# Kernel tuning notes

Hardware: AMD Instinct MI355X
Metric: run time of the kernel (lower is better)

The kernel has to match this reference:

```python
import jax, jax.numpy as jnp
import numpy as np
from jax.scipy.linalg import solve_triangular

# Production config from MFAWrapper.from_path: 28x28 images, 50 components, 6 factors
B, DFT, K, L = 2048, 784, 50, 6
LOG2PI = float(np.log(2.0 * np.pi))


def setup_inputs() -> dict:
    key = jax.random.key(0)
    k1, k2, k3, k4, k5, k6 = jax.random.split(key, 6)
    X = jax.random.normal(k1, (B, DFT), dtype=jnp.float32)
    J = jax.random.randint(k2, (B, DFT), 0, 2).astype(jnp.int32)  # binary observation mask
    MU = jax.random.normal(k3, (K, DFT), dtype=jnp.float32) * 0.5
    A_fac = jax.random.normal(k4, (K, DFT, L), dtype=jnp.float32) * 0.1  # factor loadings
    log_D = jax.random.normal(k5, (K, DFT), dtype=jnp.float32) * 0.1 - 1.0  # log noise variances
    PI_logits = jax.random.normal(k6, (K,), dtype=jnp.float32)
    return {"X": X, "J": J, "MU": MU, "A_fac": A_fac, "log_D": log_D, "PI_logits": PI_logits}


def _mfa_conditional(X, J, MU, A_fac, log_D, PI_logits):
    """Batched MFA conditional reconstruction given observed features (mask J==1).

    The per-sample torch.nonzero selection is replaced by mask-weighted linear
    algebra: restricting to observed rows of diag(1/D) is identical to zeroing
    the unobserved entries of the weight, so all B samples are conditioned in
    one batched pass instead of a Python loop.
    """
    dtype = X.dtype
    l = A_fac.shape[-1]
    Jf = (J == 1).astype(dtype)                 # [B, Dft]
    inv_D = jnp.exp(-log_D)                     # [K, Dft]
    # masked residual per (sample, component): [B, K, Dft]
    md = (X[:, None, :] - MU[None, :, :]) * Jf[:, None, :]
    # latent posterior precision P = I + A_o^T D_o^{-1} A_o  -> [B, K, L, L]
    P = jnp.einsum('bd,kd,kdi,kdj->bkij', Jf, inv_D, A_fac, A_fac) + jnp.eye(l, dtype=dtype)
    # q = A_o^T D_o^{-1} (x_o - mu_o)  -> [B, K, L]
    q = jnp.einsum('bkd,kd,kdi->bki', md, inv_D, A_fac)
    # per-component log-likelihood of observed features via Woodbury / matrix det lemma
    Lc = jnp.linalg.cholesky(P)                                         # [B, K, L, L]
    y = solve_triangular(Lc, q[..., None], lower=True)[..., 0]          # [B, K, L]
    quad = jnp.einsum('bkd,kd->bk', md * md, inv_D) - jnp.sum(y * y, axis=-1)
    logdet = (2.0 * jnp.sum(jnp.log(jnp.diagonal(Lc, axis1=-2, axis2=-1)), axis=-1)
              + jnp.einsum('bd,kd->bk', Jf, log_D))
    n_obs = jnp.sum(Jf, axis=-1, keepdims=True)                         # [B, 1]
    log_lik = -0.5 * (quad + logdet + n_obs * LOG2PI)                   # [B, K]
    log_resp = jax.nn.log_softmax(PI_logits)[None, :] + log_lik
    c = jnp.argmax(log_resp, axis=-1)                                   # most responsible component, [B]
    # gather per-sample selected component and form the conditional Gaussian in factor form
    P_sel = jnp.take_along_axis(P, c[:, None, None, None], axis=1)[:, 0]  # [B, L, L]
    q_sel = jnp.take_along_axis(q, c[:, None, None], axis=1)[:, 0]        # [B, L]
    A_sel = A_fac[c]                                                      # [B, Dft, L]
    m_z = jnp.linalg.solve(P_sel, q_sel[..., None])[..., 0]               # posterior latent mean [B, L]
    cov_z = jnp.linalg.inv(P_sel)                                         # posterior latent cov [B, L, L]
    Lz = jnp.linalg.cholesky(cov_z)
    M = MU[c] + jnp.einsum('bdi,bi->bd', A_sel, m_z)                      # conditional mean over all features
    A_out = jnp.einsum('bdi,bij->bdj', A_sel, Lz)                         # loadings: cond cov = A_out A_out^T + diag(D_out)
    D_out = jnp.exp(log_D)[c]                                             # [B, Dft]
    Pw = jnp.ones((X.shape[0], 1), dtype)
    return Pw, M, A_out, D_out


def reference(X, J, MU, A_fac, log_D, PI_logits):
    return _mfa_conditional(X, J, MU, A_fac, log_D, PI_logits)
```

## Files before the change

kernel.cpp:

```cpp
#include <hip/hip_runtime.h>
#include <math.h>

#define B_N 2048
#define D_FT 784
#define K_N 50
#define L_N 6
#define LOG2PI_F 1.8378770664093453f

#define OUT_PW 0
#define OUT_M  (B_N)
#define OUT_A  (OUT_M + B_N*D_FT)
#define OUT_D  (OUT_A + B_N*D_FT*6)

#define WS_SCORES 0
#define WS_PQ     (WS_SCORES + K_N*B_N)
#define WS_C      (WS_PQ + K_N*27*B_N)
#define WS_MZLZ   (WS_C + B_N)
#define WS_XT     (WS_MZLZ + B_N*28)
#define WS_JBT    (WS_XT + D_FT*B_N)

#define IDX(i,j) ((i)*((i)+1)/2 + (j))

typedef float v2f __attribute__((ext_vector_type(2)));

#define PK_FMA(acc, a, b) asm("v_pk_fma_f32 %0, %1, %2, %0" : "+v"(acc) : "v"(a), "v"(b))
#define PK_MUL(dst, a, b) asm("v_pk_mul_f32 %0, %1, %2" : "=v"(dst) : "v"(a), "v"(b))
#define PK_ADD(dst, a, b) asm("v_pk_add_f32 %0, %1, %2" : "=v"(dst) : "v"(a), "v"(b))

__device__ __forceinline__ void chol6(const float* P, float* L, float* rd, float* sumlog) {
    float sl = 0.f;
    #pragma unroll
    for (int j = 0; j < 6; ++j) {
        float s = P[IDX(j,j)];
        #pragma unroll
        for (int m = 0; m < j; ++m) s -= L[IDX(j,m)] * L[IDX(j,m)];
        float d = sqrtf(s);
        L[IDX(j,j)] = d;
        float r = 1.0f / d;
        rd[j] = r;
        sl += logf(d);
        #pragma unroll
        for (int i = j + 1; i < 6; ++i) {
            float t = P[IDX(i,j)];
            #pragma unroll
            for (int m = 0; m < j; ++m) t -= L[IDX(i,m)] * L[IDX(j,m)];
            L[IDX(i,j)] = t * r;
        }
    }
    *sumlog = sl;
}

__global__ __launch_bounds__(1024) void k_transpose4(const float* __restrict__ X,
                                                     float4* __restrict__ Xt4) {
    __shared__ float4 tile[32][33];
    int tx = threadIdx.x, ty = threadIdx.y;
    int d4b = blockIdx.x * 32;
    int bb  = blockIdx.y * 32;
    int d4 = d4b + tx;
    if (d4 < D_FT / 4)
        tile[ty][tx] = *(const float4*)&X[(size_t)(bb + ty) * D_FT + d4 * 4];
    __syncthreads();
    int d4o = d4b + ty;
    if (d4o < D_FT / 4)
        Xt4[(size_t)d4o * B_N + (bb + tx)] = tile[tx][ty];
}

__global__ void k_packbits(const int* __restrict__ J, unsigned* __restrict__ JbT) {
    int t = blockIdx.x * blockDim.x + threadIdx.x;
    int b = t >> 5;
    int w = t & 31;
    if (w >= 25) return;
    int d0 = w * 32;
    int n = D_FT - d0; if (n > 32) n = 32;
    unsigned u = 0;
    for (int j = 0; j < n; ++j)
        u |= (J[(size_t)b * D_FT + d0 + j] != 0 ? 1u : 0u) << j;
    JbT[(size_t)w * B_N + b] = u;
}

__global__ __launch_bounds__(256) void k_jld(const float* __restrict__ logD,
                                             const unsigned* __restrict__ JbT,
                                             float* __restrict__ SJL) {
    __shared__ float ld[800];
    const int k  = blockIdx.x >> 3;
    const int bt = blockIdx.x & 7;
    for (int i = threadIdx.x; i < 800; i += 256)
        ld[i] = (i < D_FT) ? logD[(size_t)k * D_FT + i] : 0.f;
    __syncthreads();
    const int b = bt * 256 + threadIdx.x;
    float jl = 0.f;
    for (int w = 0; w < 25; ++w) {
        unsigned mw = JbT[(size_t)w * B_N + b];
        const float* lw = &ld[w * 32];
        #pragma unroll
        for (int dd = 0; dd < 32; ++dd)
            jl += ((mw >> dd) & 1u) ? lw[dd] : 0.f;
    }
    SJL[(size_t)k * B_N + b] = jl;
}

#define ACC_PAIR(pi, dd, x0, x1) do { \
    const float4 f0 = sm4[(size_t)(pi) * 4 + 0]; \
    const float4 f1 = sm4[(size_t)(pi) * 4 + 1]; \
    const float4 f2 = sm4[(size_t)(pi) * 4 + 2]; \
    const float4 f3 = sm4[(size_t)(pi) * 4 + 3]; \
    v2f m2;  m2.x = (float)((mw >> (dd)) & 1u); m2.y = (float)((mw >> ((dd)+1)) & 1u); \
    v2f x2;  x2.x = (x0); x2.y = (x1); \
    v2f sa2;  sa2.x = f3.x;  sa2.y = f3.y; \
    v2f nmu2; nmu2.x = f3.z; nmu2.y = f3.w; \
    v2f a0; a0.x = f0.x; a0.y = f0.y;  v2f a1; a1.x = f0.z; a1.y = f0.w; \
    v2f a2; a2.x = f1.x; a2.y = f1.y;  v2f a3; a3.x = f1.z; a3.y = f1.w; \
    v2f a4; a4.x = f2.x; a4.y = f2.y;  v2f a5; a5.x = f2.z; a5.y = f2.w; \
    v2f w2;  PK_MUL(w2, m2, sa2); \
    v2f xm2; PK_ADD(xm2, x2, nmu2); \
    v2f z2;  PK_MUL(z2, w2, xm2); \
    v2f u; \
    PK_MUL(u, m2, a0); PK_FMA(Pm2[0],  u, a0); \
    PK_MUL(u, m2, a1); PK_FMA(Pm2[1],  u, a0); PK_FMA(Pm2[2],  u, a1); \
    PK_MUL(u, m2, a2); PK_FMA(Pm2[3],  u, a0); PK_FMA(Pm2[4],  u, a1); PK_FMA(Pm2[5],  u, a2); \
    PK_MUL(u, m2, a3); PK_FMA(Pm2[6],  u, a0); PK_FMA(Pm2[7],  u, a1); PK_FMA(Pm2[8],  u, a2); PK_FMA(Pm2[9],  u, a3); \
    PK_MUL(u, m2, a4); PK_FMA(Pm2[10], u, a0); PK_FMA(Pm2[11], u, a1); PK_FMA(Pm2[12], u, a2); PK_FMA(Pm2[13], u, a3); PK_FMA(Pm2[14], u, a4); \
    PK_MUL(u, m2, a5); PK_FMA(Pm2[15], u, a0); PK_FMA(Pm2[16], u, a1); PK_FMA(Pm2[17], u, a2); PK_FMA(Pm2[18], u, a3); PK_FMA(Pm2[19], u, a4); PK_FMA(Pm2[20], u, a5); \
    PK_FMA(qv2[0], z2, a0); PK_FMA(qv2[1], z2, a1); PK_FMA(qv2[2], z2, a2); \
    PK_FMA(qv2[3], z2, a3); PK_FMA(qv2[4], z2, a4); PK_FMA(qv2[5], z2, a5); \
    PK_FMA(quad2, z2, z2); \
} while (0)

__global__ __launch_bounds__(256, 4) void k_accum(
        const float4* __restrict__ Xt4, const unsigned* __restrict__ JbT,
        const float* __restrict__ A, const float* __restrict__ MU,
        const float* __restrict__ logD, const float* __restrict__ PI,
        float* __restrict__ scores, float* __restrict__ Pq) {
    __shared__ float4 sm4[(D_FT / 2) * 4];
    float* smem = (float*)sm4;
    const int k   = blockIdx.x >> 5;
    const int tid = threadIdx.x;
    const int s   = tid & 63;
    const int h   = tid >> 6;
    const int b   = (blockIdx.x & 31) * 64 + s;

    for (int p = tid; p < D_FT / 2; p += 256) {
        const float* ar0 = A + ((size_t)k * D_FT + 2 * p) * 6;
        const float* ar1 = ar0 + 6;
        float sa0 = expf(-0.5f * logD[(size_t)k * D_FT + 2 * p]);
        float sa1 = expf(-0.5f * logD[(size_t)k * D_FT + 2 * p + 1]);
        float4 f0, f1, f2, f3;
        f0.x = sa0 * ar0[0]; f0.y = sa1 * ar1[0]; f0.z = sa0 * ar0[1]; f0.w = sa1 * ar1[1];
        f1.x = sa0 * ar0[2]; f1.y = sa1 * ar1[2]; f1.z = sa0 * ar0[3]; f1.w = sa1 * ar1[3];
        f2.x = sa0 * ar0[4]; f2.y = sa1 * ar1[4]; f2.z = sa0 * ar0[5]; f2.w = sa1 * ar1[5];
        f3.x = sa0; f3.y = sa1;
        f3.z = -MU[(size_t)k * D_FT + 2 * p];
        f3.w = -MU[(size_t)k * D_FT + 2 * p + 1];
        sm4[(size_t)p * 4 + 0] = f0;
        sm4[(size_t)p * 4 + 1] = f1;
        sm4[(size_t)p * 4 + 2] = f2;
        sm4[(size_t)p * 4 + 3] = f3;
    }
    __syncthreads();

    v2f Pm2[21], qv2[6], quad2;
    #pragma unroll
    for (int t = 0; t < 21; ++t) { Pm2[t].x = 0.f; Pm2[t].y = 0.f; }
    #pragma unroll
    for (int t = 0; t < 6; ++t) { qv2[t].x = 0.f; qv2[t].y = 0.f; }
    quad2.x = 0.f; quad2.y = 0.f;
    int nob = 0;

    const int w0 = h * 6;
    const int w1 = w0 + 6;
    for (int w = w0; w < w1; ++w) {
        const unsigned mw = JbT[(size_t)w * B_N + b];
        nob += __popc(mw);
        const int wpair = w * 16;
        const float4* xp = Xt4 + (size_t)(w * 8) * B_N + b;
        #pragma unroll 2
        for (int g = 0; g < 8; ++g) {
            float4 xv = xp[(size_t)g * B_N];
            ACC_PAIR(wpair + 2 * g,     g * 4,     xv.x, xv.y);
            ACC_PAIR(wpair + 2 * g + 1, g * 4 + 2, xv.z, xv.w);
        }
    }
    if (h == 3) {
        const unsigned mw = JbT[(size_t)24 * B_N + b];
        nob += __popc(mw);
        const int wpair = 24 * 16;
        const float4* xp = Xt4 + (size_t)(24 * 8) * B_N + b;
        #pragma unroll
        for (int g = 0; g < 4; ++g) {
            float4 xv = xp[(size_t)g * B_N];
            ACC_PAIR(wpair + 2 * g,     g * 4,     xv.x, xv.y);
            ACC_PAIR(wpair + 2 * g + 1, g * 4 + 2, xv.z, xv.w);
        }
    }

    float Pm[21], qv[6], quad;
    #pragma unroll
    for (int t = 0; t < 21; ++t) Pm[t] = Pm2[t].x + Pm2[t].y;
    #pragma unroll
    for (int t = 0; t < 6; ++t) qv[t] = qv2[t].x + qv2[t].y;
    quad = quad2.x + quad2.y;

    __syncthreads();
    float* red = smem;
    if (h & 1) {
        float* o = &red[(size_t)(h >> 1) * (64 * 33) + s * 33];
        #pragma unroll
        for (int t = 0; t < 21; ++t) o[t] = Pm[t];
        #pragma unroll
        for (int t = 0; t < 6; ++t) o[21 + t] = qv[t];
        o[27] = quad; o[28] = (float)nob;
    }
    __syncthreads();
    if (!(h & 1)) {
        const float* o = &red[(size_t)(h >> 1) * (64 * 33) + s * 33];
        #pragma unroll
        for (int t = 0; t < 21; ++t) Pm[t] += o[t];
        #pragma unroll
        for (int t = 0; t < 6; ++t) qv[t] += o[21 + t];
        quad += o[27]; nob += (int)o[28];
    }
    __syncthreads();
    if (h == 2) {
        float* o = &red[s * 33];
        #pragma unroll
        for (int t = 0; t < 21; ++t) o[t] = Pm[t];
        #pragma unroll
        for (int t = 0; t < 6; ++t) o[21 + t] = qv[t];
        o[27] = quad; o[28] = (float)nob;
    }
    __syncthreads();
    if (h == 0) {
        const float* o = &red[s * 33];
        #pragma unroll
        for (int t = 0; t < 21; ++t) Pm[t] += o[t];
        #pragma unroll
        for (int t = 0; t < 6; ++t) qv[t] += o[21 + t];
        quad += o[27];
        float nobs = (float)(nob + (int)o[28]);

        float jld = scores[(size_t)k * B_N + b];

        Pm[0] += 1.f; Pm[2] += 1.f; Pm[5] += 1.f; Pm[9] += 1.f; Pm[14] += 1.f; Pm[20] += 1.f;

        float Lm[21], rd[6], sumlog;
        chol6(Pm, Lm, rd, &sumlog);
        float y[6];
        #pragma unroll
        for (int j = 0; j < 6; ++j) {
            float sv = qv[j];
            #pragma unroll
            for (int m = 0; m < j; ++m) sv -= Lm[IDX(j,m)] * y[m];
            y[j] = sv * rd[j];
        }
        float yy = 0.f;
        #pragma unroll
        for (int j = 0; j < 6; ++j) yy += y[j] * y[j];
        float logdet = 2.f * sumlog + jld;
        float ll = -0.5f * ((quad - yy) + logdet + nobs * LOG2PI_F);
        float score = ll + PI[k];

        scores[(size_t)k * B_N + b] = score;
        float* pq = Pq + (size_t)k * 27 * B_N + b;
        #pragma unroll
        for (int t = 0; t < 21; ++t) pq[(size_t)t * B_N] = Pm[t];
        #pragma unroll
        for (int t = 0; t < 6; ++t) pq[(size_t)(21 + t) * B_N] = qv[t];
    }
}

__global__ void k_select(const float* __restrict__ scores, const float* __restrict__ Pq,
                         int* __restrict__ csel, float* __restrict__ mzLz,
                         float* __restrict__ out) {
    int b = blockIdx.x * blockDim.x + threadIdx.x;
    if (b >= B_N) return;

    float best = scores[b];
    int bc = 0;
    for (int k = 1; k < K_N; ++k) {
        float s = scores[(size_t)k * B_N + b];
        if (s > best) { best = s; bc = k; }
    }
    csel[b] = bc;
    out[OUT_PW + b] = 1.0f;

    float Pm[21], qv[6];
    const float* pq = Pq + (size_t)bc * 27 * B_N + b;
    #pragma unroll
    for (int t = 0; t < 21; ++t) Pm[t] = pq[(size_t)t * B_N];
    #pragma unroll
    for (int t = 0; t < 6; ++t) qv[t] = pq[(size_t)(21 + t) * B_N];

    float Lm[21], rd[6], dummy;
    chol6(Pm, Lm, rd, &dummy);

    float y[6];
    #pragma unroll
    for (int j = 0; j < 6; ++j) {
        float s = qv[j];
        #pragma unroll
        for (int m = 0; m < j; ++m) s -= Lm[IDX(j,m)] * y[m];
        y[j] = s * rd[j];
    }
    float mz[6];
    #pragma unroll
    for (int ii = 5; ii >= 0; --ii) {
        float s = y[ii];
        #pragma unroll
        for (int j = ii + 1; j < 6; ++j) s -= Lm[IDX(j,ii)] * mz[j];
        mz[ii] = s * rd[ii];
    }
    float Li[21];
    #pragma unroll
    for (int j = 0; j < 6; ++j) {
        Li[IDX(j,j)] = rd[j];
        #pragma unroll
        for (int i = j + 1; i < 6; ++i) {
            float s = 0.f;
            #pragma unroll
            for (int m = j; m < i; ++m) s += Lm[IDX(i,m)] * Li[IDX(m,j)];
            Li[IDX(i,j)] = -s * rd[i];
        }
    }
    float cov[21];
    #pragma unroll
    for (int i = 0; i < 6; ++i) {
        #pragma unroll
        for (int j = 0; j <= i; ++j) {
            float s = 0.f;
            #pragma unroll
            for (int m = i; m < 6; ++m) s += Li[IDX(m,i)] * Li[IDX(m,j)];
            cov[IDX(i,j)] = s;
        }
    }
    float Lz[21], rd2[6];
    chol6(cov, Lz, rd2, &dummy);

    float* o = mzLz + (size_t)b * 28;
    #pragma unroll
    for (int t = 0; t < 6; ++t) o[t] = mz[t];
    #pragma unroll
    for (int t = 0; t < 21; ++t) o[6 + t] = Lz[t];
}

__global__ __launch_bounds__(256) void k_output(
        const float* __restrict__ A, const float* __restrict__ MU,
        const float* __restrict__ logD, const int* __restrict__ csel,
        const float* __restrict__ mzLz, float* __restrict__ out) {
    __shared__ float smz[6];
    __shared__ float sLz[21];
    __shared__ int sc;
    int b = blockIdx.x;
    if (threadIdx.x == 0) sc = csel[b];
    if (threadIdx.x < 27) {
        float v = mzLz[(size_t)b * 28 + threadIdx.x];
        if (threadIdx.x < 6) smz[threadIdx.x] = v;
        else sLz[threadIdx.x - 6] = v;
    }
    __syncthreads();
    int c = sc;

    for (int d = threadIdx.x; d < D_FT; d += 256) {
        const float* ar = A + ((size_t)c * D_FT + d) * 6;
        float a[6];
        #pragma unroll
        for (int i = 0; i < 6; ++i) a[i] = ar[i];
        float mu = MU[(size_t)c * D_FT + d];
        float ld = logD[(size_t)c * D_FT + d];
        float m = mu;
        #pragma unroll
        for (int i = 0; i < 6; ++i) m += a[i] * smz[i];
        out[OUT_M + (size_t)b * D_FT + d] = m;
        out[OUT_D + (size_t)b * D_FT + d] = expf(ld);
        float* ao = out + OUT_A + ((size_t)b * D_FT + d) * 6;
        #pragma unroll
        for (int j = 0; j < 6; ++j) {
            float s = 0.f;
            #pragma unroll
            for (int i = j; i < 6; ++i) s += a[i] * sLz[IDX(i,j)];
            ao[j] = s;
        }
    }
}

extern "C" void kernel_launch(void* const* d_in, const int* in_sizes, int n_in,
                              void* d_out, int out_size, void* d_ws, size_t ws_size,
                              hipStream_t stream) {
    (void)in_sizes; (void)n_in; (void)out_size; (void)ws_size;
    const float* X    = (const float*)d_in[0];
    const int*   J    = (const int*)d_in[1];
    const float* MU   = (const float*)d_in[2];
    const float* A    = (const float*)d_in[3];
    const float* logD = (const float*)d_in[4];
    const float* PI   = (const float*)d_in[5];
    float* out = (float*)d_out;
    float* ws  = (float*)d_ws;

    float*    scores = ws + WS_SCORES;
    float*    Pq     = ws + WS_PQ;
    int*      csel   = (int*)(ws + WS_C);
    float*    mzLz   = ws + WS_MZLZ;
    float4*   Xt4    = (float4*)(ws + WS_XT);
    unsigned* JbT    = (unsigned*)(ws + WS_JBT);

    dim3 g0((D_FT / 4 + 31) / 32, B_N / 32), b0(32, 32);
    k_transpose4<<<g0, b0, 0, stream>>>(X, Xt4);

    k_packbits<<<(B_N * 32) / 256, 256, 0, stream>>>(J, JbT);

    k_jld<<<K_N * 8, 256, 0, stream>>>(logD, JbT, scores);

    k_accum<<<32 * K_N, 256, 0, stream>>>(Xt4, JbT, A, MU, logD, PI, scores, Pq);

    k_select<<<B_N / 256, 256, 0, stream>>>(scores, Pq, csel, mzLz, out);

    k_output<<<B_N, 256, 0, stream>>>(A, MU, logD, csel, mzLz, out);
}
```

Before: 139.0 us.

## Precompute scaled component records in a separate kernel and read them from global memory

Moves the per-component construction of scaled loadings, inverse-sqrt noise and negated means out of every k_accum block into a small k_buildrec kernel that writes the records to workspace once. k_accum now reads those records straight from global memory (uniform across the wavefront, so effectively broadcast/scalar-cached) instead of staging 25 KB in LDS. This frees shared memory for higher occupancy and avoids recomputing expf per block. The reduction is rewritten as a serial single-slab exchange, and the packed inner math uses compiler vector ops with u*u products. The trade-offs are an extra launch and reliance on cache for the record reads.

After: 165.1 us. 18.7% more time.

```diff
diff --git a/kernel.cpp b/kernel.cpp
--- a/kernel.cpp
+++ b/kernel.cpp
@@ -18,14 +18,13 @@
 #define WS_MZLZ   (WS_C + B_N)
 #define WS_XT     (WS_MZLZ + B_N*28)
 #define WS_JBT    (WS_XT + D_FT*B_N)
+#define WS_WREC   (WS_JBT + 25*B_N)
 
 #define IDX(i,j) ((i)*((i)+1)/2 + (j))
 
 typedef float v2f __attribute__((ext_vector_type(2)));
 
 #define PK_FMA(acc, a, b) asm("v_pk_fma_f32 %0, %1, %2, %0" : "+v"(acc) : "v"(a), "v"(b))
-#define PK_MUL(dst, a, b) asm("v_pk_mul_f32 %0, %1, %2" : "=v"(dst) : "v"(a), "v"(b))
-#define PK_ADD(dst, a, b) asm("v_pk_add_f32 %0, %1, %2" : "=v"(dst) : "v"(a), "v"(b))
 
 __device__ __forceinline__ void chol6(const float* P, float* L, float* rd, float* sumlog) {
     float sl = 0.f;
@@ -99,47 +98,11 @@
     SJL[(size_t)k * B_N + b] = jl;
 }
 
-#define ACC_PAIR(pi, dd, x0, x1) do { \
-    const float4 f0 = sm4[(size_t)(pi) * 4 + 0]; \
-    const float4 f1 = sm4[(size_t)(pi) * 4 + 1]; \
-    const float4 f2 = sm4[(size_t)(pi) * 4 + 2]; \
-    const float4 f3 = sm4[(size_t)(pi) * 4 + 3]; \
-    v2f m2;  m2.x = (float)((mw >> (dd)) & 1u); m2.y = (float)((mw >> ((dd)+1)) & 1u); \
-    v2f x2;  x2.x = (x0); x2.y = (x1); \
-    v2f sa2;  sa2.x = f3.x;  sa2.y = f3.y; \
-    v2f nmu2; nmu2.x = f3.z; nmu2.y = f3.w; \
-    v2f a0; a0.x = f0.x; a0.y = f0.y;  v2f a1; a1.x = f0.z; a1.y = f0.w; \
-    v2f a2; a2.x = f1.x; a2.y = f1.y;  v2f a3; a3.x = f1.z; a3.y = f1.w; \
-    v2f a4; a4.x = f2.x; a4.y = f2.y;  v2f a5; a5.x = f2.z; a5.y = f2.w; \
-    v2f w2;  PK_MUL(w2, m2, sa2); \
-    v2f xm2; PK_ADD(xm2, x2, nmu2); \
-    v2f z2;  PK_MUL(z2, w2, xm2); \
-    v2f u; \
-    PK_MUL(u, m2, a0); PK_FMA(Pm2[0],  u, a0); \
-    PK_MUL(u, m2, a1); PK_FMA(Pm2[1],  u, a0); PK_FMA(Pm2[2],  u, a1); \
-    PK_MUL(u, m2, a2); PK_FMA(Pm2[3],  u, a0); PK_FMA(Pm2[4],  u, a1); PK_FMA(Pm2[5],  u, a2); \
-    PK_MUL(u, m2, a3); PK_FMA(Pm2[6],  u, a0); PK_FMA(Pm2[7],  u, a1); PK_FMA(Pm2[8],  u, a2); PK_FMA(Pm2[9],  u, a3); \
-    PK_MUL(u, m2, a4); PK_FMA(Pm2[10], u, a0); PK_FMA(Pm2[11], u, a1); PK_FMA(Pm2[12], u, a2); PK_FMA(Pm2[13], u, a3); PK_FMA(Pm2[14], u, a4); \
-    PK_MUL(u, m2, a5); PK_FMA(Pm2[15], u, a0); PK_FMA(Pm2[16], u, a1); PK_FMA(Pm2[17], u, a2); PK_FMA(Pm2[18], u, a3); PK_FMA(Pm2[19], u, a4); PK_FMA(Pm2[20], u, a5); \
-    PK_FMA(qv2[0], z2, a0); PK_FMA(qv2[1], z2, a1); PK_FMA(qv2[2], z2, a2); \
-    PK_FMA(qv2[3], z2, a3); PK_FMA(qv2[4], z2, a4); PK_FMA(qv2[5], z2, a5); \
-    PK_FMA(quad2, z2, z2); \
-} while (0)
-
-__global__ __launch_bounds__(256, 4) void k_accum(
-        const float4* __restrict__ Xt4, const unsigned* __restrict__ JbT,
+__global__ __launch_bounds__(256) void k_buildrec(
         const float* __restrict__ A, const float* __restrict__ MU,
-        const float* __restrict__ logD, const float* __restrict__ PI,
-        float* __restrict__ scores, float* __restrict__ Pq) {
-    __shared__ float4 sm4[(D_FT / 2) * 4];
-    float* smem = (float*)sm4;
-    const int k   = blockIdx.x >> 5;
-    const int tid = threadIdx.x;
-    const int s   = tid & 63;
-    const int h   = tid >> 6;
-    const int b   = (blockIdx.x & 31) * 64 + s;
-
-    for (int p = tid; p < D_FT / 2; p += 256) {
+        const float* __restrict__ logD, float4* __restrict__ Wrec) {
+    const int k = blockIdx.x;
+    for (int p = threadIdx.x; p < D_FT / 2; p += 256) {
         const float* ar0 = A + ((size_t)k * D_FT + 2 * p) * 6;
         const float* ar1 = ar0 + 6;
         float sa0 = expf(-0.5f * logD[(size_t)k * D_FT + 2 * p]);
@@ -151,12 +114,50 @@
         f3.x = sa0; f3.y = sa1;
         f3.z = -MU[(size_t)k * D_FT + 2 * p];
         f3.w = -MU[(size_t)k * D_FT + 2 * p + 1];
-        sm4[(size_t)p * 4 + 0] = f0;
-        sm4[(size_t)p * 4 + 1] = f1;
-        sm4[(size_t)p * 4 + 2] = f2;
-        sm4[(size_t)p * 4 + 3] = f3;
-    }
-    __syncthreads();
+        float4* w = Wrec + ((size_t)k * (D_FT / 2) + p) * 4;
+        w[0] = f0; w[1] = f1; w[2] = f2; w[3] = f3;
+    }
+}
+
+#define ACC_PAIR(pi, dd, x0, x1) do { \
+    const float4 f0 = Wr[(size_t)(pi) * 4 + 0]; \
+    const float4 f1 = Wr[(size_t)(pi) * 4 + 1]; \
+    const float4 f2 = Wr[(size_t)(pi) * 4 + 2]; \
+    const float4 f3 = Wr[(size_t)(pi) * 4 + 3]; \
+    v2f m2;  m2.x = (float)((mw >> (dd)) & 1u); m2.y = (float)((mw >> ((dd)+1)) & 1u); \
+    v2f x2;  x2.x = (x0); x2.y = (x1); \
+    v2f sa2;  sa2.x = f3.x;  sa2.y = f3.y; \
+    v2f nmu2; nmu2.x = f3.z; nmu2.y = f3.w; \
+    v2f xm2 = x2 + nmu2; \
+    v2f w2  = m2 * sa2; \
+    v2f z2  = w2 * xm2; \
+    v2f a0; a0.x = f0.x; a0.y = f0.y;  v2f a1; a1.x = f0.z; a1.y = f0.w; \
+    v2f a2; a2.x = f1.x; a2.y = f1.y;  v2f a3; a3.x = f1.z; a3.y = f1.w; \
+    v2f a4; a4.x = f2.x; a4.y = f2.y;  v2f a5; a5.x = f2.z; a5.y = f2.w; \
+    v2f u0 = m2 * a0, u1 = m2 * a1, u2 = m2 * a2; \
+    v2f u3 = m2 * a3, u4 = m2 * a4, u5 = m2 * a5; \
+    PK_FMA(Pm2[0],  u0, u0); \
+    PK_FMA(Pm2[1],  u1, u0); PK_FMA(Pm2[2],  u1, u1); \
+    PK_FMA(Pm2[3],  u2, u0); PK_FMA(Pm2[4],  u2, u1); PK_FMA(Pm2[5],  u2, u2); \
+    PK_FMA(Pm2[6],  u3, u0); PK_FMA(Pm2[7],  u3, u1); PK_FMA(Pm2[8],  u3, u2); PK_FMA(Pm2[9],  u3, u3); \
+    PK_FMA(Pm2[10], u4, u0); PK_FMA(Pm2[11], u4, u1); PK_FMA(Pm2[12], u4, u2); PK_FMA(Pm2[13], u4, u3); PK_FMA(Pm2[14], u4, u4); \
+    PK_FMA(Pm2[15], u5, u0); PK_FMA(Pm2[16], u5, u1); PK_FMA(Pm2[17], u5, u2); PK_FMA(Pm2[18], u5, u3); PK_FMA(Pm2[19], u5, u4); PK_FMA(Pm2[20], u5, u5); \
+    PK_FMA(qv2[0], z2, u0); PK_FMA(qv2[1], z2, u1); PK_FMA(qv2[2], z2, u2); \
+    PK_FMA(qv2[3], z2, u3); PK_FMA(qv2[4], z2, u4); PK_FMA(qv2[5], z2, u5); \
+    PK_FMA(quad2, z2, z2); \
+} while (0)
+
+__global__ __launch_bounds__(256, 4) void k_accum(
+        const float4* __restrict__ Xt4, const unsigned* __restrict__ JbT,
+        const float4* __restrict__ Wrec, const float* __restrict__ PI,
+        float* __restrict__ scores, float* __restrict__ Pq) {
+    __shared__ float red[64 * 33];
+    const int k   = blockIdx.x >> 5;
+    const int tid = threadIdx.x;
+    const int s   = tid & 63;
+    const int h   = tid >> 6;
+    const int b   = (blockIdx.x & 31) * 64 + s;
+    const float4* __restrict__ Wr = Wrec + (size_t)k * (D_FT / 2) * 4;
 
     v2f Pm2[21], qv2[6], quad2;
     #pragma unroll
@@ -200,43 +201,28 @@
     for (int t = 0; t < 6; ++t) qv[t] = qv2[t].x + qv2[t].y;
     quad = quad2.x + quad2.y;
 
-    __syncthreads();
-    float* red = smem;
-    if (h & 1) {
-        float* o = &red[(size_t)(h >> 1) * (64 * 33) + s * 33];
-        #pragma unroll
-        for (int t = 0; t < 21; ++t) o[t] = Pm[t];
-        #pragma unroll
-        for (int t = 0; t < 6; ++t) o[21 + t] = qv[t];
-        o[27] = quad; o[28] = (float)nob;
-    }
-    __syncthreads();
-    if (!(h & 1)) {
-        const float* o = &red[(size_t)(h >> 1) * (64 * 33) + s * 33];
-        #pragma unroll
-        for (int t = 0; t < 21; ++t) Pm[t] += o[t];
-        #pragma unroll
-        for (int t = 0; t < 6; ++t) qv[t] += o[21 + t];
-        quad += o[27]; nob += (int)o[28];
-    }
-    __syncthreads();
-    if (h == 2) {
-        float* o = &red[s * 33];
-        #pragma unroll
-        for (int t = 0; t < 21; ++t) o[t] = Pm[t];
-        #pragma unroll
-        for (int t = 0; t < 6; ++t) o[21 + t] = qv[t];
-        o[27] = quad; o[28] = (float)nob;
-    }
+    #define SLAB_WR do { float* o = &red[s * 33]; \
+        _Pragma("unroll") for (int t = 0; t < 21; ++t) o[t] = Pm[t]; \
+        _Pragma("unroll") for (int t = 0; t < 6; ++t) o[21 + t] = qv[t]; \
+        o[27] = quad; o[28] = (float)nob; } while (0)
+    #define SLAB_ADD do { const float* o = &red[s * 33]; \
+        _Pragma("unroll") for (int t = 0; t < 21; ++t) Pm[t] += o[t]; \
+        _Pragma("unroll") for (int t = 0; t < 6; ++t) qv[t] += o[21 + t]; \
+        quad += o[27]; nob += (int)o[28]; } while (0)
+
+    if (h == 1) SLAB_WR;
+    __syncthreads();
+    if (h == 0) SLAB_ADD;
+    __syncthreads();
+    if (h == 3) SLAB_WR;
+    __syncthreads();
+    if (h == 2) SLAB_ADD;
+    __syncthreads();
+    if (h == 2) SLAB_WR;
     __syncthreads();
     if (h == 0) {
-        const float* o = &red[s * 33];
-        #pragma unroll
-        for (int t = 0; t < 21; ++t) Pm[t] += o[t];
-        #pragma unroll
-        for (int t = 0; t < 6; ++t) qv[t] += o[21 + t];
-        quad += o[27];
-        float nobs = (float)(nob + (int)o[28]);
+        SLAB_ADD;
+        float nobs = (float)nob;
 
         float jld = scores[(size_t)k * B_N + b];
 
@@ -401,6 +387,7 @@
     float*    mzLz   = ws + WS_MZLZ;
     float4*   Xt4    = (float4*)(ws + WS_XT);
     unsigned* JbT    = (unsigned*)(ws + WS_JBT);
+    float4*   Wrec   = (float4*)(ws + WS_WREC);
 
     dim3 g0((D_FT / 4 + 31) / 32, B_N / 32), b0(32, 32);
     k_transpose4<<<g0, b0, 0, stream>>>(X, Xt4);
@@ -409,7 +396,9 @@
 
     k_jld<<<K_N * 8, 256, 0, stream>>>(logD, JbT, scores);
 
-    k_accum<<<32 * K_N, 256, 0, stream>>>(Xt4, JbT, A, MU, logD, PI, scores, Pq);
+    k_buildrec<<<K_N, 256, 0, stream>>>(A, MU, logD, Wrec);
+
+    k_accum<<<32 * K_N, 256, 0, stream>>>(Xt4, JbT, Wrec, PI, scores, Pq);
 
     k_select<<<B_N / 256, 256, 0, stream>>>(scores, Pq, csel, mzLz, out);
 
```
